# Optimization experiments

Measured on AMD Instinct MI355X. Metric: run time of the kernel, lower is better.

## Reference

```python
import jax, jax.numpy as jnp
import numpy as np

N_HIDDEN = 32
RANK = 6
SV_DECAY_GAMMA = 0.3
LEAK_ALPHA = 0.1
INPUT_DIM = 64
OUTPUT_DIM = 32


def setup_inputs() -> dict:
    key = jax.random.key(0)
    ks = jax.random.split(key, 8)
    B, T = 256, 2048
    inputs = jax.random.normal(ks[0], (B, T, INPUT_DIM), dtype=jnp.float32)
    # parameters (match torch init scales)
    m = jax.random.normal(ks[1], (N_HIDDEN, 1), dtype=jnp.float32) * 0.1
    n = jax.random.normal(ks[2], (N_HIDDEN, 1), dtype=jnp.float32) * 0.1
    M = jax.random.normal(ks[3], (N_HIDDEN, RANK), dtype=jnp.float32) * 0.1
    Nmat = jax.random.normal(ks[4], (N_HIDDEN, RANK), dtype=jnp.float32) * 0.1
    # singular-value-decay scaling of M, N (as in _initialize_with_sv_decay)
    target_sv = jnp.exp(-SV_DECAY_GAMMA * jnp.arange(RANK, dtype=jnp.float32))
    target_sv = target_sv / target_sv.sum() * RANK
    sqrt_sv = jnp.sqrt(target_sv)
    M = M * sqrt_sv[None, :]
    Nmat = Nmat * sqrt_sv[None, :]
    bias = jnp.zeros((N_HIDDEN,), dtype=jnp.float32)
    # W_in: Linear(input_dim, N, bias=False) -> weight [N, input_dim]
    lim_in = 1.0 / np.sqrt(INPUT_DIM)
    W_in = jax.random.uniform(ks[5], (N_HIDDEN, INPUT_DIM), minval=-lim_in, maxval=lim_in, dtype=jnp.float32)
    lim_out = 1.0 / np.sqrt(N_HIDDEN)
    W_out = jax.random.uniform(ks[6], (OUTPUT_DIM, N_HIDDEN), minval=-lim_out, maxval=lim_out, dtype=jnp.float32)
    b_out = jax.random.uniform(ks[7], (OUTPUT_DIM,), minval=-lim_out, maxval=lim_out, dtype=jnp.float32)
    return {"inputs": inputs, "W_in": W_in, "m": m, "n": n, "M": M,
            "Nmat": Nmat, "bias": bias, "W_out": W_out, "b_out": b_out}


def reference(inputs, W_in, m, n, M, Nmat, bias, W_out, b_out):
    # h_{t+1} = (1-a) h_t + a * tanh(W_rec h_t + W_in u_t + b); y_t = W_out h_t + b_out
    B, T, _ = inputs.shape
    alpha = LEAK_ALPHA
    # W_rec = m n^T + M N^T (time-invariant; torch recomputes per step, same math)
    W_rec = m @ n.T + M @ Nmat.T                         # [N, N]
    x_proj = jnp.einsum('bti,ni->btn', inputs, W_in)     # [B, T, N]
    h0 = jnp.zeros((B, N_HIDDEN), dtype=inputs.dtype)

    def step(h, x_t):
        pre = h @ W_rec.T + x_t + bias
        h_new = (1.0 - alpha) * h + alpha * jnp.tanh(pre)
        return h_new, h_new

    h_final, hs = jax.lax.scan(step, h0, jnp.swapaxes(x_proj, 0, 1))  # hs: [T, B, N]
    outputs = jnp.einsum('tbn,on->bto', hs, W_out) + b_out            # [B, T, O]
    return outputs, h_final
```

## Files before the change

kernel.cpp:

```cpp
#include <hip/hip_runtime.h>

#define RNN_B 256
#define RNN_T 2048
#define RNN_IN 64
#define RNN_N 32
#define RNN_O 32
#define RNN_R 6
#define RNN_ALPHA 0.1f
#define KSCALE 2.8853900817779268f

__global__ __launch_bounds__(256) void k_xproj(
    const float* __restrict__ u, const float* __restrict__ W_in,
    const float* __restrict__ bias, float* __restrict__ xp)
{
    __shared__ float4 lds[4096];
    const int tid = threadIdx.x;
    const size_t row0 = (size_t)blockIdx.x * 256;

    const float4* __restrict__ u4 =
        reinterpret_cast<const float4*>(u) + row0 * (RNN_IN / 4);
    #pragma unroll
    for (int j = 0; j < 16; ++j) {
        const int g   = tid + j * 256;
        const int row = g >> 4, q = g & 15;
        lds[row * 16 + (q ^ (row & 15))] = u4[g];
    }
    __syncthreads();

    float acc[RNN_N];
    #pragma unroll
    for (int n = 0; n < RNN_N; ++n) acc[n] = bias[n];
    const int sw = tid & 15;
    #pragma unroll
    for (int qq = 0; qq < RNN_IN / 4; ++qq) {
        const float4 v = lds[tid * 16 + (qq ^ sw)];
        #pragma unroll
        for (int n = 0; n < RNN_N; ++n) {
            const float* wr = W_in + n * RNN_IN + 4 * qq;
            acc[n] = fmaf(wr[0], v.x, acc[n]);
            acc[n] = fmaf(wr[1], v.y, acc[n]);
            acc[n] = fmaf(wr[2], v.z, acc[n]);
            acc[n] = fmaf(wr[3], v.w, acc[n]);
        }
    }
    __syncthreads();

    const int sw8 = tid & 7;
    #pragma unroll
    for (int q = 0; q < RNN_N / 4; ++q)
        lds[tid * 8 + (q ^ sw8)] =
            make_float4(KSCALE * acc[4*q+0], KSCALE * acc[4*q+1],
                        KSCALE * acc[4*q+2], KSCALE * acc[4*q+3]);
    __syncthreads();

    float4* __restrict__ o4 =
        reinterpret_cast<float4*>(xp) + row0 * (RNN_N / 4);
    #pragma unroll
    for (int j = 0; j < 8; ++j) {
        const int g   = tid + j * 256;
        const int row = g >> 3, q = g & 7;
        o4[g] = lds[row * 8 + (q ^ (row & 7))];
    }
}

template <int CTRL>
__device__ __forceinline__ float dpp_add(float v) {
    int t = __builtin_amdgcn_update_dpp(0, __float_as_int(v), CTRL, 0xf, 0xf, true);
    return v + __int_as_float(t);
}
__device__ __forceinline__ float xsum32(float v) {
#if __has_builtin(__builtin_amdgcn_permlane32_swap)
    typedef int v2i __attribute__((ext_vector_type(2)));
    v2i r = __builtin_amdgcn_permlane32_swap(__float_as_int(v),
                                             __float_as_int(v), false, false);
    return __int_as_float(r.x) + __int_as_float(r.y);
#else
    return v + __shfl_xor(v, 32, 64);
#endif
}
__device__ __forceinline__ float xsum16(float v) {
#if __has_builtin(__builtin_amdgcn_permlane16_swap)
    typedef int v2i __attribute__((ext_vector_type(2)));
    v2i r = __builtin_amdgcn_permlane16_swap(__float_as_int(v),
                                             __float_as_int(v), false, false);
    return __int_as_float(r.x) + __int_as_float(r.y);
#else
    return v + __shfl_xor(v, 16, 64);
#endif
}
__device__ __forceinline__ float fast_exp2(float x) {
#if __has_builtin(__builtin_amdgcn_exp2f)
    return __builtin_amdgcn_exp2f(x);
#else
    return __expf(x * 0.6931471805599453f);
#endif
}
__device__ __forceinline__ float fast_rcp(float x) {
#if __has_builtin(__builtin_amdgcn_rcpf)
    return __builtin_amdgcn_rcpf(x);
#else
    return __frcp_rn(x);
#endif
}

__global__ __launch_bounds__(64, 1) void k_recur(
    const float* __restrict__ m, const float* __restrict__ nvec,
    const float* __restrict__ Mmat, const float* __restrict__ Nmat,
    const float* __restrict__ xp,
    float* __restrict__ hout,
    float* __restrict__ hfin)
{
    const int b    = blockIdx.x;
    const int lane = threadIdx.x;
    const int k    = lane & 15;
    const int q    = (lane >> 4) & 1;
    const int p    = lane >> 5;
    const int e    = 2 * k + p;

    float cn[4], cm[4];
    #pragma unroll
    for (int j = 0; j < 4; ++j) {
        const int r = 4 * q + j;
        float cnv = 0.f, cmv = 0.f;
        if (r == 0)          { cnv = nvec[e];               cmv = m[e]; }
        else if (r <= RNN_R) { cnv = Nmat[e*RNN_R + (r-1)]; cmv = Mmat[e*RNN_R + (r-1)]; }
        cn[j] = cnv;
        cm[j] = KSCALE * cmv;
    }

    const float2* __restrict__ x2 =
        reinterpret_cast<const float2*>(xp + (size_t)b * (RNN_T * RNN_N)) + k;
    float* __restrict__ hbase = hout + (size_t)b * (RNN_T * RNN_N);

    float h = 0.0f;

    const int PF = 8;
    float2 xr[PF];
    #pragma unroll
    for (int i = 0; i < PF; ++i) xr[i] = x2[i * (RNN_N / 2)];

    const bool do_store = (q == 0);

    #pragma unroll 8
    for (int t = 0; t < RNN_T; ++t) {
        const int slot = t & (PF - 1);
        const float2 xv = xr[slot];
        xr[slot] = x2[(t + PF) * (RNN_N / 2)];
        const float xe = p ? xv.y : xv.x;

        float s0 = cn[0] * h, s1 = cn[1] * h, s2 = cn[2] * h, s3 = cn[3] * h;
        s0 = dpp_add<0xB1>(s0);  s1 = dpp_add<0xB1>(s1);
        s2 = dpp_add<0xB1>(s2);  s3 = dpp_add<0xB1>(s3);
        s0 = dpp_add<0x4E>(s0);  s1 = dpp_add<0x4E>(s1);
        s2 = dpp_add<0x4E>(s2);  s3 = dpp_add<0x4E>(s3);
        s0 = dpp_add<0x141>(s0); s1 = dpp_add<0x141>(s1);
        s2 = dpp_add<0x141>(s2); s3 = dpp_add<0x141>(s3);
        s0 = dpp_add<0x140>(s0); s1 = dpp_add<0x140>(s1);
        s2 = dpp_add<0x140>(s2); s3 = dpp_add<0x140>(s3);

        s0 = xsum32(s0); s1 = xsum32(s1); s2 = xsum32(s2); s3 = xsum32(s3);

        float w = fmaf(cm[1], s1, cm[0] * s0) + fmaf(cm[3], s3, cm[2] * s2);
        w = xsum16(w);
        const float z = w + xe;

        const float ez = fast_exp2(z);
        const float g  = fmaf(1.0f - RNN_ALPHA, h, RNN_ALPHA);
        h = fmaf(-2.0f * RNN_ALPHA, fast_rcp(ez + 1.0f), g);

        if (do_store) hbase[t * RNN_N + e] = h;
    }
    if (do_store) hfin[b * RNN_N + e] = h;
}

__global__ __launch_bounds__(256) void k_out(
    const float* __restrict__ W_out, const float* __restrict__ b_out,
    const float* __restrict__ hsrc, float* __restrict__ ydst)
{
    __shared__ float4 lds[2048];
    const int tid = threadIdx.x;
    const size_t row0 = (size_t)blockIdx.x * 256;

    const float4* __restrict__ h4 =
        reinterpret_cast<const float4*>(hsrc) + row0 * (RNN_N / 4);
    #pragma unroll
    for (int j = 0; j < 8; ++j) {
        const int g   = tid + j * 256;
        const int row = g >> 3, q = g & 7;
        lds[row * 8 + (q ^ (row & 7))] = h4[g];
    }
    __syncthreads();

    float y[RNN_O];
    #pragma unroll
    for (int o = 0; o < RNN_O; ++o) y[o] = b_out[o];
    const int sw = tid & 7;
    #pragma unroll
    for (int qq = 0; qq < RNN_N / 4; ++qq) {
        const float4 v = lds[tid * 8 + (qq ^ sw)];
        #pragma unroll
        for (int o = 0; o < RNN_O; ++o) {
            const float* wr = W_out + o * RNN_N + 4 * qq;
            y[o] = fmaf(wr[0], v.x, y[o]);
            y[o] = fmaf(wr[1], v.y, y[o]);
            y[o] = fmaf(wr[2], v.z, y[o]);
            y[o] = fmaf(wr[3], v.w, y[o]);
        }
    }
    __syncthreads();

    #pragma unroll
    for (int q = 0; q < RNN_O / 4; ++q)
        lds[tid * 8 + (q ^ sw)] =
            make_float4(y[4*q+0], y[4*q+1], y[4*q+2], y[4*q+3]);
    __syncthreads();

    float4* __restrict__ o4 =
        reinterpret_cast<float4*>(ydst) + row0 * (RNN_O / 4);
    #pragma unroll
    for (int j = 0; j < 8; ++j) {
        const int g   = tid + j * 256;
        const int row = g >> 3, q = g & 7;
        o4[g] = lds[row * 8 + (q ^ (row & 7))];
    }
}

extern "C" void kernel_launch(void* const* d_in, const int* in_sizes, int n_in,
                              void* d_out, int out_size, void* d_ws, size_t ws_size,
                              hipStream_t stream)
{
    const float* u     = (const float*)d_in[0];
    const float* W_in  = (const float*)d_in[1];
    const float* m     = (const float*)d_in[2];
    const float* nvec  = (const float*)d_in[3];
    const float* Mmat  = (const float*)d_in[4];
    const float* Nmat  = (const float*)d_in[5];
    const float* bias  = (const float*)d_in[6];
    const float* W_out = (const float*)d_in[7];
    const float* b_out = (const float*)d_in[8];
    float* out = (float*)d_out;

    float* hfin = out + (size_t)RNN_B * RNN_T * RNN_N;

    const size_t hbytes = (size_t)RNN_B * RNN_T * RNN_N * sizeof(float);
    float* hbuf = (ws_size >= hbytes) ? (float*)d_ws : out;

    k_xproj<<<(RNN_B * RNN_T) / 256, 256, 0, stream>>>(u, W_in, bias, out);
    k_recur<<<RNN_B, 64, 0, stream>>>(m, nvec, Mmat, Nmat, out, hbuf, hfin);
    k_out  <<<(RNN_B * RNN_T) / 256, 256, 0, stream>>>(W_out, b_out, hbuf, out);
}
```

Baseline: 615.6 us.

## Fuse output projection into recurrence kernel via LDS double-buffered hidden state

Removes the separate output-projection kernel. Each step now writes h into a double-buffered LDS array, and the recurrent wavefront computes y for the previous timestep from it with a 16-FMA partial dot plus a cross-half sum, storing y directly. This avoids writing and re-reading the full hidden-state history through global memory and drops one launch. In exchange it adds LDS traffic and FMAs to the latency-critical serial loop. It also relies on wavefront-synchronous LDS ordering with no barrier between steps.

```diff
diff --git a/kernel.cpp b/kernel.cpp
--- a/kernel.cpp
+++ b/kernel.cpp
@@ -106,10 +106,12 @@
 __global__ __launch_bounds__(64, 1) void k_recur(
     const float* __restrict__ m, const float* __restrict__ nvec,
     const float* __restrict__ Mmat, const float* __restrict__ Nmat,
+    const float* __restrict__ W_out, const float* __restrict__ b_out,
     const float* __restrict__ xp,
-    float* __restrict__ hout,
+    float* __restrict__ yout,
     float* __restrict__ hfin)
 {
+    __shared__ float hbuf[2][RNN_N];
     const int b    = blockIdx.x;
     const int lane = threadIdx.x;
     const int k    = lane & 15;
@@ -128,18 +130,30 @@
         cm[j] = KSCALE * cmv;
     }
 
+    const int o = lane & 31;
+    const int z = p;
+    float4 wo0, wo1, wo2, wo3;
+    {
+        const float4* wrow =
+            reinterpret_cast<const float4*>(W_out + o * RNN_N + 16 * z);
+        wo0 = wrow[0]; wo1 = wrow[1]; wo2 = wrow[2]; wo3 = wrow[3];
+    }
+    const float ybias = (z == 0) ? b_out[o] : 0.0f;
+
     const float2* __restrict__ x2 =
         reinterpret_cast<const float2*>(xp + (size_t)b * (RNN_T * RNN_N)) + k;
-    float* __restrict__ hbase = hout + (size_t)b * (RNN_T * RNN_N);
+    float* __restrict__ ybase = yout + (size_t)b * (RNN_T * RNN_N);
 
     float h = 0.0f;
+    if (q == 0) { hbuf[0][e] = 0.f; hbuf[1][e] = 0.f; }
 
     const int PF = 8;
     float2 xr[PF];
     #pragma unroll
     for (int i = 0; i < PF; ++i) xr[i] = x2[i * (RNN_N / 2)];
 
-    const bool do_store = (q == 0);
+    const bool hwrite = (q == 0);
+    const bool ystore = (p == 0);
 
     #pragma unroll 8
     for (int t = 0; t < RNN_T; ++t) {
@@ -147,6 +161,11 @@
         const float2 xv = xr[slot];
         xr[slot] = x2[(t + PF) * (RNN_N / 2)];
         const float xe = p ? xv.y : xv.x;
+
+        const float4* hprev =
+            reinterpret_cast<const float4*>(&hbuf[(t + 1) & 1][16 * z]);
+        const float4 a0 = hprev[0], a1 = hprev[1],
+                     a2 = hprev[2], a3 = hprev[3];
 
         float s0 = cn[0] * h, s1 = cn[1] * h, s2 = cn[2] * h, s3 = cn[3] * h;
         s0 = dpp_add<0xB1>(s0);  s1 = dpp_add<0xB1>(s1);
@@ -162,67 +181,46 @@
 
         float w = fmaf(cm[1], s1, cm[0] * s0) + fmaf(cm[3], s3, cm[2] * s2);
         w = xsum16(w);
-        const float z = w + xe;
-
-        const float ez = fast_exp2(z);
+        const float zz = w + xe;
+
+        const float ez = fast_exp2(zz);
         const float g  = fmaf(1.0f - RNN_ALPHA, h, RNN_ALPHA);
         h = fmaf(-2.0f * RNN_ALPHA, fast_rcp(ez + 1.0f), g);
 
-        if (do_store) hbase[t * RNN_N + e] = h;
-    }
-    if (do_store) hfin[b * RNN_N + e] = h;
-}
-
-__global__ __launch_bounds__(256) void k_out(
-    const float* __restrict__ W_out, const float* __restrict__ b_out,
-    const float* __restrict__ hsrc, float* __restrict__ ydst)
-{
-    __shared__ float4 lds[2048];
-    const int tid = threadIdx.x;
-    const size_t row0 = (size_t)blockIdx.x * 256;
-
-    const float4* __restrict__ h4 =
-        reinterpret_cast<const float4*>(hsrc) + row0 * (RNN_N / 4);
-    #pragma unroll
-    for (int j = 0; j < 8; ++j) {
-        const int g   = tid + j * 256;
-        const int row = g >> 3, q = g & 7;
-        lds[row * 8 + (q ^ (row & 7))] = h4[g];
-    }
-    __syncthreads();
-
-    float y[RNN_O];
-    #pragma unroll
-    for (int o = 0; o < RNN_O; ++o) y[o] = b_out[o];
-    const int sw = tid & 7;
-    #pragma unroll
-    for (int qq = 0; qq < RNN_N / 4; ++qq) {
-        const float4 v = lds[tid * 8 + (qq ^ sw)];
-        #pragma unroll
-        for (int o = 0; o < RNN_O; ++o) {
-            const float* wr = W_out + o * RNN_N + 4 * qq;
-            y[o] = fmaf(wr[0], v.x, y[o]);
-            y[o] = fmaf(wr[1], v.y, y[o]);
-            y[o] = fmaf(wr[2], v.z, y[o]);
-            y[o] = fmaf(wr[3], v.w, y[o]);
-        }
-    }
-    __syncthreads();
-
-    #pragma unroll
-    for (int q = 0; q < RNN_O / 4; ++q)
-        lds[tid * 8 + (q ^ sw)] =
-            make_float4(y[4*q+0], y[4*q+1], y[4*q+2], y[4*q+3]);
-    __syncthreads();
-
-    float4* __restrict__ o4 =
-        reinterpret_cast<float4*>(ydst) + row0 * (RNN_O / 4);
-    #pragma unroll
-    for (int j = 0; j < 8; ++j) {
-        const int g   = tid + j * 256;
-        const int row = g >> 3, q = g & 7;
-        o4[g] = lds[row * 8 + (q ^ (row & 7))];
-    }
+        if (hwrite) hbuf[t & 1][e] = h;
+
+        float yp = ybias;
+        yp = fmaf(wo0.x, a0.x, yp); yp = fmaf(wo0.y, a0.y, yp);
+        yp = fmaf(wo0.z, a0.z, yp); yp = fmaf(wo0.w, a0.w, yp);
+        yp = fmaf(wo1.x, a1.x, yp); yp = fmaf(wo1.y, a1.y, yp);
+        yp = fmaf(wo1.z, a1.z, yp); yp = fmaf(wo1.w, a1.w, yp);
+        yp = fmaf(wo2.x, a2.x, yp); yp = fmaf(wo2.y, a2.y, yp);
+        yp = fmaf(wo2.z, a2.z, yp); yp = fmaf(wo2.w, a2.w, yp);
+        yp = fmaf(wo3.x, a3.x, yp); yp = fmaf(wo3.y, a3.y, yp);
+        yp = fmaf(wo3.z, a3.z, yp); yp = fmaf(wo3.w, a3.w, yp);
+        const float yv = xsum32(yp);
+        if (t >= 1 && ystore) ybase[(size_t)(t - 1) * RNN_N + o] = yv;
+    }
+
+    {
+        const float4* hprev =
+            reinterpret_cast<const float4*>(&hbuf[(RNN_T - 1) & 1][16 * z]);
+        const float4 a0 = hprev[0], a1 = hprev[1],
+                     a2 = hprev[2], a3 = hprev[3];
+        float yp = ybias;
+        yp = fmaf(wo0.x, a0.x, yp); yp = fmaf(wo0.y, a0.y, yp);
+        yp = fmaf(wo0.z, a0.z, yp); yp = fmaf(wo0.w, a0.w, yp);
+        yp = fmaf(wo1.x, a1.x, yp); yp = fmaf(wo1.y, a1.y, yp);
+        yp = fmaf(wo1.z, a1.z, yp); yp = fmaf(wo1.w, a1.w, yp);
+        yp = fmaf(wo2.x, a2.x, yp); yp = fmaf(wo2.y, a2.y, yp);
+        yp = fmaf(wo2.z, a2.z, yp); yp = fmaf(wo2.w, a2.w, yp);
+        yp = fmaf(wo3.x, a3.x, yp); yp = fmaf(wo3.y, a3.y, yp);
+        yp = fmaf(wo3.z, a3.z, yp); yp = fmaf(wo3.w, a3.w, yp);
+        const float yv = xsum32(yp);
+        if (ystore) ybase[(size_t)(RNN_T - 1) * RNN_N + o] = yv;
+    }
+
+    if (hwrite) hfin[b * RNN_N + e] = h;
 }
 
 extern "C" void kernel_launch(void* const* d_in, const int* in_sizes, int n_in,
@@ -242,10 +240,10 @@
 
     float* hfin = out + (size_t)RNN_B * RNN_T * RNN_N;
 
-    const size_t hbytes = (size_t)RNN_B * RNN_T * RNN_N * sizeof(float);
-    float* hbuf = (ws_size >= hbytes) ? (float*)d_ws : out;
-
-    k_xproj<<<(RNN_B * RNN_T) / 256, 256, 0, stream>>>(u, W_in, bias, out);
-    k_recur<<<RNN_B, 64, 0, stream>>>(m, nvec, Mmat, Nmat, out, hbuf, hfin);
-    k_out  <<<(RNN_B * RNN_T) / 256, 256, 0, stream>>>(W_out, b_out, hbuf, out);
-}
+    const size_t xpbytes = (size_t)RNN_B * RNN_T * RNN_N * sizeof(float);
+    float* xpbuf = (ws_size >= xpbytes) ? (float*)d_ws : out;
+
+    k_xproj<<<(RNN_B * RNN_T) / 256, 256, 0, stream>>>(u, W_in, bias, xpbuf);
+    k_recur<<<RNN_B, 64, 0, stream>>>(m, nvec, Mmat, Nmat, W_out, b_out,
+                                      xpbuf, out, hfin);
+}
```

Result: slower. 687.0 us (+11.6%).
